# Performance work log

Measured on AMD Instinct MI355X. Metric: run time of the kernel, lower is better.

Reference implementation:

```python
import jax, jax.numpy as jnp
import numpy as np

NUM_HEADS = 16
HEAD_DIM = 64  # d_model // num_heads = 1024 // 16
NUM_BUCKETS = 20


def setup_inputs() -> dict:
    key = jax.random.key(0)
    ks = jax.random.split(key, 5)
    B, S, D = 2, 2048, 1024
    v = jax.random.normal(ks[0], (B, S, D), dtype=jnp.float32)
    k = jax.random.normal(ks[1], (B, S, D), dtype=jnp.float32)
    q = jax.random.normal(ks[2], (B, S, D), dtype=jnp.float32)
    mask = jax.random.randint(ks[3], (B, S, S), 0, 2).astype(jnp.bool_)
    diff_matrix = jax.random.randint(ks[4], (B, S, S), 0, NUM_BUCKETS)
    rel_bias = jax.random.normal(jax.random.fold_in(key, 7), (NUM_BUCKETS, NUM_HEADS), dtype=jnp.float32)
    return {"v": v, "k": k, "q": q, "mask": mask, "diff_matrix": diff_matrix, "rel_bias": rel_bias}


def _split_heads(x):
    B, S, _ = x.shape
    return x.reshape(B, S, NUM_HEADS, HEAD_DIM).transpose(0, 2, 1, 3)  # [B,H,S,hd]


def reference(v, k, q, mask, diff_matrix, rel_bias):
    B, S, D = q.shape
    qh, kh, vh = _split_heads(q), _split_heads(k), _split_heads(v)
    scale = 1.0 / jnp.sqrt(jnp.float32(HEAD_DIM))
    scores = jnp.einsum('bhqd,bhkd->bhqk', qh, kh) * scale  # [B,H,S,S]
    # relative bias: gather [B,S,S,H] -> [B,H,S,S]
    bias = rel_bias[diff_matrix].transpose(0, 3, 1, 2)
    att = jax.nn.silu(scores + bias)
    att = jnp.where(mask[:, None, :, :], att, 0.0)
    av = jnp.einsum('bhqk,bhkd->bhqd', att, vh)  # [B,H,S,hd]
    return av.transpose(0, 2, 1, 3).reshape(B, S, D)
```

## Files before the change

kernel.cpp:

```cpp
#include <hip/hip_runtime.h>
#include <hip/hip_fp16.h>
#include <cstdint>
#include <cstddef>

#define SEQ 2048
#define DM 1024
#define NH 16
#define NB 20

typedef _Float16 half8 __attribute__((ext_vector_type(8)));
typedef _Float16 half4 __attribute__((ext_vector_type(4)));
typedef _Float16 h2v __attribute__((ext_vector_type(2)));
typedef float f32x4 __attribute__((ext_vector_type(4)));
typedef int i32x4 __attribute__((ext_vector_type(4)));
typedef unsigned int u32;
typedef unsigned int u32x2 __attribute__((ext_vector_type(2)));

#define KF_HALVES 4194304
#define VF_HALVES 4194304

__global__ __launch_bounds__(256) void pa_prep(
    const float* __restrict__ v, const float* __restrict__ k,
    const int* __restrict__ diff, const int* __restrict__ mask,
    _Float16* __restrict__ KF, _Float16* __restrict__ VF,
    unsigned char* __restrict__ PB) {
  const int bid = blockIdx.x, tid = threadIdx.x;
  if (bid < 2048) {
    int img = bid >> 4;
    int bb = img >> 6, kt = img & 63;
    int tix = ((bid & 15) << 8) | tid;
    int r = tix >> 7;
    int c0 = (tix & 127) << 3;
    const float* src = k + ((size_t)(bb * SEQ + kt * 32 + r)) * DM + c0;
    f32x4 a = *(const f32x4*)src;
    f32x4 c = *(const f32x4*)(src + 4);
    half8 o = {(_Float16)a[0], (_Float16)a[1], (_Float16)a[2], (_Float16)a[3],
               (_Float16)c[0], (_Float16)c[1], (_Float16)c[2], (_Float16)c[3]};
    int h = c0 >> 6, dh = (c0 >> 5) & 1, g4 = (c0 >> 3) & 3;
    int k2 = r >> 4, l16 = r & 15;
    int lane = g4 * 16 + l16;
    size_t off = ((size_t)((bb * 16 + h) * 64 + kt)) * 2048 + (k2 * 2 + dh) * 512 + lane * 8;
    *(half8*)(KF + off) = o;
  } else if (bid < 3072) {
    int b3 = bid - 2048;
    int img = b3 >> 3;
    int bb = img >> 6, kt = img & 63;
    int tix = ((b3 & 7) << 8) | tid;
    int kq = tix >> 8;
    int k2 = kq >> 2, g4 = kq & 3;
    int d0 = (tix & 255) << 2;
    const float* src = v + ((size_t)(bb * SEQ + kt * 32 + k2 * 16 + g4 * 4)) * DM + d0;
    f32x4 m0 = *(const f32x4*)(src);
    f32x4 m1 = *(const f32x4*)(src + DM);
    f32x4 m2 = *(const f32x4*)(src + 2 * DM);
    f32x4 m3 = *(const f32x4*)(src + 3 * DM);
#pragma unroll
    for (int i = 0; i < 4; ++i) {
      int d = d0 + i;
      int l16 = d & 15, dt = (d >> 4) & 3, dtp = dt >> 1, w = dt & 1, h = d >> 6;
      int lane = g4 * 16 + l16;
      half4 o = {(_Float16)m0[i], (_Float16)m1[i], (_Float16)m2[i], (_Float16)m3[i]};
      size_t off = ((size_t)((bb * 16 + h) * 64 + kt)) * 2048 + (k2 * 2 + dtp) * 512 + lane * 8 + w * 4;
      *(half4*)(VF + off) = o;
    }
  } else {
    int b4 = bid - 3072;
    int job = b4 >> 5;
    int bb = job >> 6, qblk = job & 63;
    int tix = ((b4 & 31) << 8) | tid;
    int kt = tix >> 7;
    int rem = tix & 127;
    int g4 = rem & 3, l16 = (rem >> 2) & 15, qs = rem >> 6;
    int lane = g4 * 16 + l16;
    int qrow = qblk * 32 + qs * 16 + l16;
    size_t rowbase = ((size_t)(bb * SEQ + qrow)) * SEQ;
    u32x2 wds;
#pragma unroll
    for (int k2 = 0; k2 < 2; ++k2) {
      int kk = kt * 32 + k2 * 16 + g4 * 4;
      i32x4 dv = *(const i32x4*)(diff + rowbase + kk);
      i32x4 mv = *(const i32x4*)(mask + rowbase + kk);
      u32 wd = 0;
#pragma unroll
      for (int r = 0; r < 4; ++r) {
        u32 byte = mv[r] ? ((u32)dv[r] << 2) : 80u;
        wd |= byte << (8 * r);
      }
      wds[k2] = wd;
    }
    size_t off = ((size_t)job) * 65536 + (size_t)kt * 1024 + (size_t)lane * 16 + (size_t)qs * 8;
    *(u32x2*)(PB + off) = wds;
  }
}

__device__ __forceinline__ half4 silu4b(const f32x4& s, h2v b01, h2v b23) {
  h2v x01 = __builtin_bit_cast(h2v, __builtin_amdgcn_cvt_pkrtz(s[0], s[1])) + b01;
  h2v x23 = __builtin_bit_cast(h2v, __builtin_amdgcn_cvt_pkrtz(s[2], s[3])) + b23;
  const h2v NL2E = {(_Float16)-1.44269504f, (_Float16)-1.44269504f};
  const h2v ONE = {(_Float16)1.0f, (_Float16)1.0f};
  h2v m01 = x01 * NL2E, m23 = x23 * NL2E;
  h2v e01 = __builtin_bit_cast(h2v, h2exp2(__builtin_bit_cast(__half2, m01)));
  h2v e23 = __builtin_bit_cast(h2v, h2exp2(__builtin_bit_cast(__half2, m23)));
  h2v d01 = e01 + ONE, d23 = e23 + ONE;
  h2v y01 = x01 * __builtin_bit_cast(h2v, h2rcp(__builtin_bit_cast(__half2, d01)));
  h2v y23 = x23 * __builtin_bit_cast(h2v, h2rcp(__builtin_bit_cast(__half2, d23)));
  return (half4){y01[0], y01[1], y23[0], y23[1]};
}

struct BiasSet { h2v b[2][2][2]; };

__device__ __forceinline__ void gather_bias(BiasSet& bs, const i32x4& pq, int rbi) {
#pragma unroll
  for (int qs = 0; qs < 2; ++qs)
#pragma unroll
    for (int k2 = 0; k2 < 2; ++k2) {
      u32 u = (u32)pq[qs * 2 + k2];
      float b0 = __int_as_float(__builtin_amdgcn_ds_bpermute((int)(u & 0xffu), rbi));
      float b1 = __int_as_float(__builtin_amdgcn_ds_bpermute((int)((u >> 8) & 0xffu), rbi));
      float b2 = __int_as_float(__builtin_amdgcn_ds_bpermute((int)((u >> 16) & 0xffu), rbi));
      float b3 = __int_as_float(__builtin_amdgcn_ds_bpermute((int)(u >> 24), rbi));
      bs.b[qs][k2][0] = __builtin_bit_cast(h2v, __builtin_amdgcn_cvt_pkrtz(b0, b1));
      bs.b[qs][k2][1] = __builtin_bit_cast(h2v, __builtin_amdgcn_cvt_pkrtz(b2, b3));
    }
}

__device__ __forceinline__ void compute_tile(
    const half8 (&kfr)[4], const half8 (&vvr)[4], const BiasSet& bs,
    const half8 (&qf)[2][2], f32x4 (&acc)[2][4]) {
  const f32x4 zf = {0.f, 0.f, 0.f, 0.f};
#pragma unroll
  for (int k2 = 0; k2 < 2; ++k2) {
    f32x4 sa[2];
#pragma unroll
    for (int qs = 0; qs < 2; ++qs) {
      sa[qs] = __builtin_amdgcn_mfma_f32_16x16x32_f16(kfr[k2 * 2 + 0], qf[qs][0], zf, 0, 0, 0);
      sa[qs] = __builtin_amdgcn_mfma_f32_16x16x32_f16(kfr[k2 * 2 + 1], qf[qs][1], sa[qs], 0, 0, 0);
    }
    half4 pf[2];
    pf[0] = silu4b(sa[0], bs.b[0][k2][0], bs.b[0][k2][1]);
    pf[1] = silu4b(sa[1], bs.b[1][k2][0], bs.b[1][k2][1]);

    half4 vf0 = __builtin_shufflevector(vvr[k2 * 2 + 0], vvr[k2 * 2 + 0], 0, 1, 2, 3);
    half4 vf1 = __builtin_shufflevector(vvr[k2 * 2 + 0], vvr[k2 * 2 + 0], 4, 5, 6, 7);
    half4 vf2 = __builtin_shufflevector(vvr[k2 * 2 + 1], vvr[k2 * 2 + 1], 0, 1, 2, 3);
    half4 vf3 = __builtin_shufflevector(vvr[k2 * 2 + 1], vvr[k2 * 2 + 1], 4, 5, 6, 7);
#pragma unroll
    for (int qs = 0; qs < 2; ++qs) {
      acc[qs][0] = __builtin_amdgcn_mfma_f32_16x16x16f16(pf[qs], vf0, acc[qs][0], 0, 0, 0);
      acc[qs][1] = __builtin_amdgcn_mfma_f32_16x16x16f16(pf[qs], vf1, acc[qs][1], 0, 0, 0);
      acc[qs][2] = __builtin_amdgcn_mfma_f32_16x16x16f16(pf[qs], vf2, acc[qs][2], 0, 0, 0);
      acc[qs][3] = __builtin_amdgcn_mfma_f32_16x16x16f16(pf[qs], vf3, acc[qs][3], 0, 0, 0);
    }
  }
}

__global__ __launch_bounds__(256, 3) void pa_main(
    const _Float16* __restrict__ KF, const _Float16* __restrict__ VF,
    const unsigned char* __restrict__ PB, const float* __restrict__ q,
    const float* __restrict__ relbias, float* __restrict__ out) {
  const int tid = threadIdx.x, lane = tid & 63, wid = tid >> 6;
  const int l16 = lane & 15, g4 = lane >> 4;
  const int L = (blockIdx.x & 7) * 128 + (blockIdx.x >> 3);
  const int h = L & 15;
  const int qgrp = (L >> 4) & 15;
  const int ksp = (L >> 8) & 1;
  const int b = L >> 9;
  const int qblk = qgrp * 4 + wid;
  const int qbase = qblk * 32;

  const float rbv = (lane < NB) ? relbias[lane * NH + h] : -30000.0f;
  const int rbi = __float_as_int(rbv);

  half8 qf[2][2];
#pragma unroll
  for (int qs = 0; qs < 2; ++qs)
#pragma unroll
    for (int dh = 0; dh < 2; ++dh) {
      const float* s = q + ((size_t)(b * SEQ + qbase + qs * 16 + l16)) * DM + h * 64 + dh * 32 + g4 * 8;
      f32x4 a = *(const f32x4*)s;
      f32x4 c = *(const f32x4*)(s + 4);
      qf[qs][dh] = {(_Float16)(a[0] * 0.125f), (_Float16)(a[1] * 0.125f),
                    (_Float16)(a[2] * 0.125f), (_Float16)(a[3] * 0.125f),
                    (_Float16)(c[0] * 0.125f), (_Float16)(c[1] * 0.125f),
                    (_Float16)(c[2] * 0.125f), (_Float16)(c[3] * 0.125f)};
    }

  f32x4 acc[2][4];
#pragma unroll
  for (int qs = 0; qs < 2; ++qs)
#pragma unroll
    for (int dt = 0; dt < 4; ++dt) acc[qs][dt] = (f32x4){0.f, 0.f, 0.f, 0.f};

  const _Float16* kfb = KF + ((size_t)((b * 16 + h) * 64 + ksp * 32)) * 2048 + lane * 8;
  const _Float16* vfb = VF + ((size_t)((b * 16 + h) * 64 + ksp * 32)) * 2048 + lane * 8;
  const unsigned char* pbb = PB + ((size_t)(b * 64 + qblk)) * 65536 + (size_t)(ksp * 32) * 1024 + lane * 16;

#define LOADKV(T, KR, VR)                                              \
  do {                                                                 \
    _Pragma("unroll") for (int j = 0; j < 4; ++j) {                    \
      KR[j] = *(const half8*)(kfb + (size_t)(T) * 2048 + j * 512);     \
      VR[j] = *(const half8*)(vfb + (size_t)(T) * 2048 + j * 512);     \
    }                                                                  \
  } while (0)
#define CLMP(T) ((T) < 32 ? (T) : 31)

  half8 kA[4], vA[4], kB[4], vB[4];
  i32x4 pq1, pqX;
  BiasSet biasA, biasB;

  LOADKV(0, kA, vA);
  {
    i32x4 pqP = *(const i32x4*)(pbb);
    gather_bias(biasA, pqP, rbi);
  }
  pq1 = *(const i32x4*)(pbb + 1024);

  for (int t = 0; t < 32; t += 2) {
    LOADKV(t + 1, kB, vB);
    pqX = *(const i32x4*)(pbb + (size_t)CLMP(t + 2) * 1024);
    __builtin_amdgcn_sched_barrier(0);
    gather_bias(biasB, pq1, rbi);
    compute_tile(kA, vA, biasA, qf, acc);
    LOADKV(CLMP(t + 2), kA, vA);
    pq1 = *(const i32x4*)(pbb + (size_t)CLMP(t + 3) * 1024);
    __builtin_amdgcn_sched_barrier(0);
    gather_bias(biasA, pqX, rbi);
    compute_tile(kB, vB, biasB, qf, acc);
  }
#undef LOADKV
#undef CLMP

#pragma unroll
  for (int qs = 0; qs < 2; ++qs)
#pragma unroll
    for (int dt = 0; dt < 4; ++dt)
#pragma unroll
      for (int r = 0; r < 4; ++r) {
        int qrow = qbase + qs * 16 + g4 * 4 + r;
        int d = h * 64 + dt * 16 + l16;
        atomicAdd(&out[((size_t)(b * SEQ) + qrow) * DM + d], acc[qs][dt][r]);
      }
}

extern "C" void kernel_launch(void* const* d_in, const int* in_sizes, int n_in,
                              void* d_out, int out_size, void* d_ws, size_t ws_size,
                              hipStream_t stream) {
  const float* v = (const float*)d_in[0];
  const float* k = (const float*)d_in[1];
  const float* q = (const float*)d_in[2];
  const int* mask = (const int*)d_in[3];
  const int* diff = (const int*)d_in[4];
  const float* relbias = (const float*)d_in[5];
  float* out = (float*)d_out;

  _Float16* KF = (_Float16*)d_ws;
  _Float16* VF = KF + KF_HALVES;
  unsigned char* PB = (unsigned char*)(VF + VF_HALVES);
  if (ws_size < (size_t)25165824) return;

  (void)hipMemsetAsync(d_out, 0, (size_t)out_size * sizeof(float), stream);
  pa_prep<<<7168, 256, 0, stream>>>(v, k, diff, mask, KF, VF, PB);
  pa_main<<<1024, 256, 0, stream>>>(KF, VF, PB, q, relbias, out);
}
```

Measured before the change: 105.0 us.

## Share K/V tiles across waves via LDS with direct global-to-LDS loads

Previously each of the four waves in a block loaded the same K and V tile from global memory into its own registers. Now each wave loads one quarter of the tile straight into a double-buffered LDS area using global_load_lds, and all waves then read the full tile from LDS, with block barriers between stages. This removes the redundant global and L2 traffic and frees the K/V prefetch registers, which is why the launch bound now asks for 4 blocks per CU instead of 3. In exchange it adds __syncthreads per tile, which can expose load latency, and correctness relies on the compiler waiting on the async LDS writes before the barrier.

New measurement: 109.7 us. 1.05x slower.

```diff
diff --git a/kernel.cpp b/kernel.cpp
--- a/kernel.cpp
+++ b/kernel.cpp
@@ -93,6 +93,12 @@
   }
 }
 
+__device__ __forceinline__ void gll16(const _Float16* g, _Float16* l) {
+  __builtin_amdgcn_global_load_lds(
+      (const __attribute__((address_space(1))) unsigned int*)g,
+      (__attribute__((address_space(3))) unsigned int*)l, 16, 0, 0);
+}
+
 __device__ __forceinline__ half4 silu4b(const f32x4& s, h2v b01, h2v b23) {
   h2v x01 = __builtin_bit_cast(h2v, __builtin_amdgcn_cvt_pkrtz(s[0], s[1])) + b01;
   h2v x23 = __builtin_bit_cast(h2v, __builtin_amdgcn_cvt_pkrtz(s[2], s[3])) + b23;
@@ -124,40 +130,13 @@
     }
 }
 
-__device__ __forceinline__ void compute_tile(
-    const half8 (&kfr)[4], const half8 (&vvr)[4], const BiasSet& bs,
-    const half8 (&qf)[2][2], f32x4 (&acc)[2][4]) {
-  const f32x4 zf = {0.f, 0.f, 0.f, 0.f};
-#pragma unroll
-  for (int k2 = 0; k2 < 2; ++k2) {
-    f32x4 sa[2];
-#pragma unroll
-    for (int qs = 0; qs < 2; ++qs) {
-      sa[qs] = __builtin_amdgcn_mfma_f32_16x16x32_f16(kfr[k2 * 2 + 0], qf[qs][0], zf, 0, 0, 0);
-      sa[qs] = __builtin_amdgcn_mfma_f32_16x16x32_f16(kfr[k2 * 2 + 1], qf[qs][1], sa[qs], 0, 0, 0);
-    }
-    half4 pf[2];
-    pf[0] = silu4b(sa[0], bs.b[0][k2][0], bs.b[0][k2][1]);
-    pf[1] = silu4b(sa[1], bs.b[1][k2][0], bs.b[1][k2][1]);
-
-    half4 vf0 = __builtin_shufflevector(vvr[k2 * 2 + 0], vvr[k2 * 2 + 0], 0, 1, 2, 3);
-    half4 vf1 = __builtin_shufflevector(vvr[k2 * 2 + 0], vvr[k2 * 2 + 0], 4, 5, 6, 7);
-    half4 vf2 = __builtin_shufflevector(vvr[k2 * 2 + 1], vvr[k2 * 2 + 1], 0, 1, 2, 3);
-    half4 vf3 = __builtin_shufflevector(vvr[k2 * 2 + 1], vvr[k2 * 2 + 1], 4, 5, 6, 7);
-#pragma unroll
-    for (int qs = 0; qs < 2; ++qs) {
-      acc[qs][0] = __builtin_amdgcn_mfma_f32_16x16x16f16(pf[qs], vf0, acc[qs][0], 0, 0, 0);
-      acc[qs][1] = __builtin_amdgcn_mfma_f32_16x16x16f16(pf[qs], vf1, acc[qs][1], 0, 0, 0);
-      acc[qs][2] = __builtin_amdgcn_mfma_f32_16x16x16f16(pf[qs], vf2, acc[qs][2], 0, 0, 0);
-      acc[qs][3] = __builtin_amdgcn_mfma_f32_16x16x16f16(pf[qs], vf3, acc[qs][3], 0, 0, 0);
-    }
-  }
-}
-
-__global__ __launch_bounds__(256, 3) void pa_main(
+__global__ __launch_bounds__(256, 4) void pa_main(
     const _Float16* __restrict__ KF, const _Float16* __restrict__ VF,
     const unsigned char* __restrict__ PB, const float* __restrict__ q,
     const float* __restrict__ relbias, float* __restrict__ out) {
+  __shared__ _Float16 ldsK[2][2048];
+  __shared__ _Float16 ldsV[2][2048];
+
   const int tid = threadIdx.x, lane = tid & 63, wid = tid >> 6;
   const int l16 = lane & 15, g4 = lane >> 4;
   const int L = (blockIdx.x & 7) * 128 + (blockIdx.x >> 3);
@@ -194,41 +173,71 @@
   const _Float16* kfb = KF + ((size_t)((b * 16 + h) * 64 + ksp * 32)) * 2048 + lane * 8;
   const _Float16* vfb = VF + ((size_t)((b * 16 + h) * 64 + ksp * 32)) * 2048 + lane * 8;
   const unsigned char* pbb = PB + ((size_t)(b * 64 + qblk)) * 65536 + (size_t)(ksp * 32) * 1024 + lane * 16;
-
-#define LOADKV(T, KR, VR)                                              \
-  do {                                                                 \
-    _Pragma("unroll") for (int j = 0; j < 4; ++j) {                    \
-      KR[j] = *(const half8*)(kfb + (size_t)(T) * 2048 + j * 512);     \
-      VR[j] = *(const half8*)(vfb + (size_t)(T) * 2048 + j * 512);     \
-    }                                                                  \
+  const int c512 = wid * 512;
+
+#define STAGE(T, B)                                          \
+  do {                                                       \
+    gll16(kfb + (size_t)(T) * 2048 + c512, &ldsK[B][c512]);  \
+    gll16(vfb + (size_t)(T) * 2048 + c512, &ldsV[B][c512]);  \
   } while (0)
 #define CLMP(T) ((T) < 32 ? (T) : 31)
 
-  half8 kA[4], vA[4], kB[4], vB[4];
+#define COMPUTE(B, BS)                                                                       \
+  do {                                                                                       \
+    const f32x4 zf = {0.f, 0.f, 0.f, 0.f};                                                   \
+    half8 kfr[4], vvr[4];                                                                    \
+    _Pragma("unroll") for (int j = 0; j < 4; ++j) {                                          \
+      kfr[j] = *(const half8*)&ldsK[B][j * 512 + lane * 8];                                  \
+      vvr[j] = *(const half8*)&ldsV[B][j * 512 + lane * 8];                                  \
+    }                                                                                        \
+    _Pragma("unroll") for (int k2 = 0; k2 < 2; ++k2) {                                       \
+      f32x4 sa[2];                                                                           \
+      _Pragma("unroll") for (int qs = 0; qs < 2; ++qs) {                                     \
+        sa[qs] = __builtin_amdgcn_mfma_f32_16x16x32_f16(kfr[k2 * 2 + 0], qf[qs][0], zf, 0, 0, 0); \
+        sa[qs] = __builtin_amdgcn_mfma_f32_16x16x32_f16(kfr[k2 * 2 + 1], qf[qs][1], sa[qs], 0, 0, 0); \
+      }                                                                                      \
+      half4 pf[2];                                                                           \
+      pf[0] = silu4b(sa[0], BS.b[0][k2][0], BS.b[0][k2][1]);                                 \
+      pf[1] = silu4b(sa[1], BS.b[1][k2][0], BS.b[1][k2][1]);                                 \
+      half4 vf0 = __builtin_shufflevector(vvr[k2 * 2 + 0], vvr[k2 * 2 + 0], 0, 1, 2, 3);     \
+      half4 vf1 = __builtin_shufflevector(vvr[k2 * 2 + 0], vvr[k2 * 2 + 0], 4, 5, 6, 7);     \
+      half4 vf2 = __builtin_shufflevector(vvr[k2 * 2 + 1], vvr[k2 * 2 + 1], 0, 1, 2, 3);     \
+      half4 vf3 = __builtin_shufflevector(vvr[k2 * 2 + 1], vvr[k2 * 2 + 1], 4, 5, 6, 7);     \
+      _Pragma("unroll") for (int qs = 0; qs < 2; ++qs) {                                     \
+        acc[qs][0] = __builtin_amdgcn_mfma_f32_16x16x16f16(pf[qs], vf0, acc[qs][0], 0, 0, 0); \
+        acc[qs][1] = __builtin_amdgcn_mfma_f32_16x16x16f16(pf[qs], vf1, acc[qs][1], 0, 0, 0); \
+        acc[qs][2] = __builtin_amdgcn_mfma_f32_16x16x16f16(pf[qs], vf2, acc[qs][2], 0, 0, 0); \
+        acc[qs][3] = __builtin_amdgcn_mfma_f32_16x16x16f16(pf[qs], vf3, acc[qs][3], 0, 0, 0); \
+      }                                                                                      \
+    }                                                                                        \
+  } while (0)
+
+  BiasSet biasA, biasB;
   i32x4 pq1, pqX;
-  BiasSet biasA, biasB;
-
-  LOADKV(0, kA, vA);
-  {
-    i32x4 pqP = *(const i32x4*)(pbb);
-    gather_bias(biasA, pqP, rbi);
-  }
+
+  STAGE(0, 0);
+  i32x4 pq0 = *(const i32x4*)(pbb);
   pq1 = *(const i32x4*)(pbb + 1024);
+  __syncthreads();
+  gather_bias(biasA, pq0, rbi);
 
   for (int t = 0; t < 32; t += 2) {
-    LOADKV(t + 1, kB, vB);
+    STAGE(t + 1, 1);
     pqX = *(const i32x4*)(pbb + (size_t)CLMP(t + 2) * 1024);
     __builtin_amdgcn_sched_barrier(0);
     gather_bias(biasB, pq1, rbi);
-    compute_tile(kA, vA, biasA, qf, acc);
-    LOADKV(CLMP(t + 2), kA, vA);
+    COMPUTE(0, biasA);
+    __syncthreads();
+    STAGE(CLMP(t + 2), 0);
     pq1 = *(const i32x4*)(pbb + (size_t)CLMP(t + 3) * 1024);
     __builtin_amdgcn_sched_barrier(0);
     gather_bias(biasA, pqX, rbi);
-    compute_tile(kB, vB, biasB, qf, acc);
+    COMPUTE(1, biasB);
+    __syncthreads();
   }
-#undef LOADKV
+#undef STAGE
 #undef CLMP
+#undef COMPUTE
 
 #pragma unroll
   for (int qs = 0; qs < 2; ++qs)
```
